# Performance work log

Measured on AMD Instinct MI355X. Metric: run time of the kernel, lower is better.

Reference implementation:

```python
import jax, jax.numpy as jnp
import numpy as np

NUM_CATEGORIES = 64
INPUT_DIM = 256
HIDDEN_DIM = 256
N = 4096  # number of samples (each with its own category)
M = 16    # rows per sample


def setup_inputs() -> dict:
    key = jax.random.key(0)
    k_x, k_cat, k_W = jax.random.split(key, 3)
    x = jax.random.normal(k_x, (N, M, INPUT_DIM), dtype=jnp.float32)
    cat_ids = jax.random.randint(k_cat, (N,), 0, NUM_CATEGORIES, dtype=jnp.int64)
    W = 0.02 * jax.random.normal(k_W, (NUM_CATEGORIES, INPUT_DIM, HIDDEN_DIM), dtype=jnp.float32)
    b = jnp.zeros((NUM_CATEGORIES, HIDDEN_DIM), dtype=jnp.float32)
    return {"x": x, "cat_ids": cat_ids, "W": W, "b": b}


def reference(x, cat_ids, W, b):
    # Gather per-sample weights/biases, then batched matmul + bias add.
    selected_W = W[cat_ids]              # [N, input_dim, hidden_dim]
    selected_b = b[cat_ids]              # [N, hidden_dim]
    out = jnp.einsum('nmi,nih->nmh', x, selected_W) + selected_b[:, None, :]
    return out
```

## Files before the change

### kernel.cpp

```cpp
#include <hip/hip_runtime.h>
#include <hip/hip_bf16.h>
#include <stdint.h>

#define N_SAMPLES 4096
#define M_ROWS 16
#define K_DIM 256
#define H_DIM 256
#define N_CATS 64
#define SPB 4
#define MAX_PADDED (N_SAMPLES + N_CATS * (SPB - 1))
#define NB (MAX_PADDED / SPB)

typedef _Float16 half8 __attribute__((ext_vector_type(8)));
typedef float floatx4 __attribute__((ext_vector_type(4)));

#define WT_BYTES ((size_t)N_CATS * K_DIM * H_DIM * 2)
#define CNT_OFF  WT_BYTES
#define CUR_OFF  (CNT_OFF + 256)
#define POFF_OFF (CNT_OFF + 512)
#define ORD_OFF  (CNT_OFF + 1024)
#define WS_NEED  (ORD_OFF + (size_t)MAX_PADDED * 4)

__global__ void prep_init(int* cnt, int* cur, int* ord) {
  int i = blockIdx.x * 256 + threadIdx.x;
  if (i < N_CATS) { cnt[i] = 0; cur[i] = 0; }
  if (i < MAX_PADDED) ord[i] = -1;
}

__global__ void prep_hist(const int* __restrict__ cat, int* cnt) {
  int i = blockIdx.x * 256 + threadIdx.x;
  if (i < N_SAMPLES) atomicAdd(&cnt[cat[i]], 1);
}

__global__ void prep_scan(const int* __restrict__ cnt, int* poff) {
  if (threadIdx.x == 0) {
    int run = 0;
    for (int c = 0; c < N_CATS; c++) {
      poff[c] = run;
      run += ((cnt[c] + SPB - 1) / SPB) * SPB;
    }
    poff[N_CATS] = run;
  }
}

__global__ void prep_scatter(const int* __restrict__ cat, const int* __restrict__ poff,
                             int* cur, int* __restrict__ ord) {
  int i = blockIdx.x * 256 + threadIdx.x;
  if (i < N_SAMPLES) {
    int c = cat[i];
    int p = poff[c] + atomicAdd(&cur[c], 1);
    ord[p] = i;
  }
}

__global__ __launch_bounds__(256)
void wt_transpose(const float* __restrict__ W, _Float16* __restrict__ Wt) {
  __shared__ _Float16 t[64][72];
  const int bid = blockIdx.x;
  const int c  = bid >> 4;
  const int kb = (bid >> 2) & 3;
  const int hb = bid & 3;
  const int tid = threadIdx.x;
  const int r  = tid >> 2;
  const int cg = (tid & 3) * 16;
  const float* src = W + ((size_t)c << 16) + (size_t)(kb * 64 + r) * 256 + hb * 64 + cg;
#pragma unroll
  for (int j = 0; j < 16; j += 4) {
    float4 v = *(const float4*)(src + j);
    t[r][cg + j + 0] = (_Float16)v.x;
    t[r][cg + j + 1] = (_Float16)v.y;
    t[r][cg + j + 2] = (_Float16)v.z;
    t[r][cg + j + 3] = (_Float16)v.w;
  }
  __syncthreads();
  _Float16* dst = Wt + ((size_t)c << 16) + (size_t)(hb * 64 + r) * 256 + kb * 64 + cg;
  half8 o0, o1;
#pragma unroll
  for (int j = 0; j < 8; j++) o0[j] = t[cg + j][r];
#pragma unroll
  for (int j = 0; j < 8; j++) o1[j] = t[cg + 8 + j][r];
  *(half8*)(dst) = o0;
  *(half8*)(dst + 8) = o1;
}

__global__ __launch_bounds__(256, 4)
void gemm_kernel(const float* __restrict__ x, const int* __restrict__ cat_ids,
                 const float* __restrict__ bias, const _Float16* __restrict__ Wt,
                 const int* __restrict__ ord, float* __restrict__ out) {
  __shared__ _Float16 sA[64 * 32];
  __shared__ _Float16 sB[H_DIM * 32];
  __shared__ int s_meta[SPB];

  const int tid = threadIdx.x;
  const int b = blockIdx.x;
  if (tid < SPB) s_meta[tid] = ord[b * SPB + tid];
  __syncthreads();
  const int s0 = s_meta[0];
  if (s0 < 0) return;
  const int cat = cat_ids[s0];

  const int wid  = tid >> 6;
  const int lane = tid & 63;
  const int l15  = lane & 15;
  const int quad = lane >> 4;

  const int arow = tid >> 2;
  const int akq  = tid & 3;
  const int asmp = s_meta[arow >> 4];
  const float* asrc = (asmp >= 0)
      ? (x + ((size_t)asmp * 16 + (arow & 15)) * K_DIM + akq * 8) : nullptr;
  _Float16* adst = &sA[arow * 32 + akq * 8];

  const _Float16* wbase = Wt + ((size_t)cat << 16);

  floatx4 acc[4][4];
#pragma unroll
  for (int i = 0; i < 4; i++)
#pragma unroll
    for (int j = 0; j < 4; j++)
#pragma unroll
      for (int e = 0; e < 4; e++) acc[i][j][e] = 0.0f;

  for (int kt = 0; kt < K_DIM / 32; ++kt) {
    __syncthreads();
    if (asrc) {
      const float4* p = (const float4*)(asrc + kt * 32);
      float4 v0 = p[0], v1 = p[1];
      half8 h;
      h[0] = (_Float16)v0.x; h[1] = (_Float16)v0.y;
      h[2] = (_Float16)v0.z; h[3] = (_Float16)v0.w;
      h[4] = (_Float16)v1.x; h[5] = (_Float16)v1.y;
      h[6] = (_Float16)v1.z; h[7] = (_Float16)v1.w;
      *(half8*)adst = h;
    } else {
      half8 h;
#pragma unroll
      for (int j = 0; j < 8; j++) h[j] = (_Float16)0.0f;
      *(half8*)adst = h;
    }
#pragma unroll
    for (int i = 0; i < 4; i++) {
      const int hbase = (wid * 4 + i) * 16;
      const _Float16* g = wbase + (size_t)(hbase + (lane >> 2)) * K_DIM + kt * 32 + (lane & 3) * 8;
      __builtin_amdgcn_global_load_lds(
          (__attribute__((address_space(1))) void*)g,
          (__attribute__((address_space(3))) void*)&sB[hbase * 32], 16, 0, 0);
    }
    __syncthreads();
    half8 af[4], bf[4];
#pragma unroll
    for (int mt = 0; mt < 4; mt++)
      af[mt] = *(const half8*)&sA[(mt * 16 + l15) * 32 + quad * 8];
#pragma unroll
    for (int nt = 0; nt < 4; nt++)
      bf[nt] = *(const half8*)&sB[(wid * 64 + nt * 16 + l15) * 32 + quad * 8];
#pragma unroll
    for (int mt = 0; mt < 4; mt++)
#pragma unroll
      for (int nt = 0; nt < 4; nt++)
        acc[mt][nt] = __builtin_amdgcn_mfma_f32_16x16x32_f16(af[mt], bf[nt], acc[mt][nt], 0, 0, 0);
  }

#pragma unroll
  for (int mt = 0; mt < 4; mt++) {
    int s = s_meta[mt];
    if (s < 0) continue;
    float* obase = out + (size_t)s * 16 * H_DIM;
#pragma unroll
    for (int nt = 0; nt < 4; nt++) {
      int col = wid * 64 + nt * 16 + l15;
      float bv = bias[cat * H_DIM + col];
#pragma unroll
      for (int r = 0; r < 4; r++) {
        int row = quad * 4 + r;
        obase[(size_t)row * H_DIM + col] = acc[mt][nt][r] + bv;
      }
    }
  }
}

__global__ __launch_bounds__(256)
void naive_kernel(const float* __restrict__ x, const int* __restrict__ cat,
                  const float* __restrict__ W, const float* __restrict__ bias,
                  float* __restrict__ out) {
  __shared__ float sx[16 * 256];
  const int n = blockIdx.x;
  const int tid = threadIdx.x;
  const int c = cat[n];
  const float* xs = x + (size_t)n * 16 * 256;
  for (int i = tid; i < 16 * 256; i += 256) sx[i] = xs[i];
  __syncthreads();
  const float* Wc = W + ((size_t)c << 16);
  float accv[16];
  float bv = bias[c * 256 + tid];
#pragma unroll
  for (int m = 0; m < 16; m++) accv[m] = bv;
  for (int k = 0; k < 256; k++) {
    float w = Wc[(size_t)k * 256 + tid];
#pragma unroll
    for (int m = 0; m < 16; m++) accv[m] += sx[m * 256 + k] * w;
  }
#pragma unroll
  for (int m = 0; m < 16; m++) out[((size_t)n * 16 + m) * 256 + tid] = accv[m];
}

extern "C" void kernel_launch(void* const* d_in, const int* in_sizes, int n_in,
                              void* d_out, int out_size, void* d_ws, size_t ws_size,
                              hipStream_t stream) {
  const float* x    = (const float*)d_in[0];
  const int*   cat  = (const int*)d_in[1];
  const float* W    = (const float*)d_in[2];
  const float* bias = (const float*)d_in[3];
  float* out = (float*)d_out;

  if (ws_size < WS_NEED) {
    naive_kernel<<<N_SAMPLES, 256, 0, stream>>>(x, cat, W, bias, out);
    return;
  }

  char* ws = (char*)d_ws;
  _Float16* Wt = (_Float16*)ws;
  int* cnt  = (int*)(ws + CNT_OFF);
  int* cur  = (int*)(ws + CUR_OFF);
  int* poff = (int*)(ws + POFF_OFF);
  int* ord  = (int*)(ws + ORD_OFF);

  wt_transpose<<<N_CATS * 16, 256, 0, stream>>>(W, Wt);
  prep_init<<<(MAX_PADDED + 255) / 256, 256, 0, stream>>>(cnt, cur, ord);
  prep_hist<<<(N_SAMPLES + 255) / 256, 256, 0, stream>>>(cat, cnt);
  prep_scan<<<1, 64, 0, stream>>>(cnt, poff);
  prep_scatter<<<(N_SAMPLES + 255) / 256, 256, 0, stream>>>(cat, poff, cur, ord);
  gemm_kernel<<<NB, 256, 0, stream>>>(x, cat, bias, Wt, ord, out);
}
```

Before: 186.1 us.

## Fuse prep kernels into one launch and split GEMM output columns across blocks

```diff
diff --git a/kernel.cpp b/kernel.cpp
--- a/kernel.cpp
+++ b/kernel.cpp
@@ -9,91 +9,90 @@
 #define N_CATS 64
 #define SPB 4
 #define MAX_PADDED (N_SAMPLES + N_CATS * (SPB - 1))
-#define NB (MAX_PADDED / SPB)
+#define NGROUP (MAX_PADDED / SPB)
+#define GPX (NGROUP / 8)
+#define GEMM_GRID (NGROUP * 2)
 
 typedef _Float16 half8 __attribute__((ext_vector_type(8)));
 typedef float floatx4 __attribute__((ext_vector_type(4)));
 
 #define WT_BYTES ((size_t)N_CATS * K_DIM * H_DIM * 2)
-#define CNT_OFF  WT_BYTES
-#define CUR_OFF  (CNT_OFF + 256)
-#define POFF_OFF (CNT_OFF + 512)
-#define ORD_OFF  (CNT_OFF + 1024)
+#define ORD_OFF  WT_BYTES
 #define WS_NEED  (ORD_OFF + (size_t)MAX_PADDED * 4)
 
-__global__ void prep_init(int* cnt, int* cur, int* ord) {
-  int i = blockIdx.x * 256 + threadIdx.x;
-  if (i < N_CATS) { cnt[i] = 0; cur[i] = 0; }
-  if (i < MAX_PADDED) ord[i] = -1;
-}
-
-__global__ void prep_hist(const int* __restrict__ cat, int* cnt) {
-  int i = blockIdx.x * 256 + threadIdx.x;
-  if (i < N_SAMPLES) atomicAdd(&cnt[cat[i]], 1);
-}
-
-__global__ void prep_scan(const int* __restrict__ cnt, int* poff) {
-  if (threadIdx.x == 0) {
-    int run = 0;
-    for (int c = 0; c < N_CATS; c++) {
-      poff[c] = run;
-      run += ((cnt[c] + SPB - 1) / SPB) * SPB;
-    }
-    poff[N_CATS] = run;
-  }
-}
-
-__global__ void prep_scatter(const int* __restrict__ cat, const int* __restrict__ poff,
-                             int* cur, int* __restrict__ ord) {
-  int i = blockIdx.x * 256 + threadIdx.x;
-  if (i < N_SAMPLES) {
-    int c = cat[i];
-    int p = poff[c] + atomicAdd(&cur[c], 1);
-    ord[p] = i;
-  }
-}
-
 __global__ __launch_bounds__(256)
-void wt_transpose(const float* __restrict__ W, _Float16* __restrict__ Wt) {
-  __shared__ _Float16 t[64][72];
-  const int bid = blockIdx.x;
-  const int c  = bid >> 4;
-  const int kb = (bid >> 2) & 3;
-  const int hb = bid & 3;
+void prep_combined(const float* __restrict__ W, _Float16* __restrict__ Wt,
+                   const int* __restrict__ cat, int* __restrict__ ord) {
   const int tid = threadIdx.x;
-  const int r  = tid >> 2;
-  const int cg = (tid & 3) * 16;
-  const float* src = W + ((size_t)c << 16) + (size_t)(kb * 64 + r) * 256 + hb * 64 + cg;
-#pragma unroll
-  for (int j = 0; j < 16; j += 4) {
-    float4 v = *(const float4*)(src + j);
-    t[r][cg + j + 0] = (_Float16)v.x;
-    t[r][cg + j + 1] = (_Float16)v.y;
-    t[r][cg + j + 2] = (_Float16)v.z;
-    t[r][cg + j + 3] = (_Float16)v.w;
-  }
-  __syncthreads();
-  _Float16* dst = Wt + ((size_t)c << 16) + (size_t)(hb * 64 + r) * 256 + kb * 64 + cg;
-  half8 o0, o1;
-#pragma unroll
-  for (int j = 0; j < 8; j++) o0[j] = t[cg + j][r];
-#pragma unroll
-  for (int j = 0; j < 8; j++) o1[j] = t[cg + 8 + j][r];
-  *(half8*)(dst) = o0;
-  *(half8*)(dst + 8) = o1;
-}
-
-__global__ __launch_bounds__(256, 4)
+  if (blockIdx.x < 1024) {
+    __shared__ _Float16 t[64][72];
+    const int bid = blockIdx.x;
+    const int c  = bid >> 4;
+    const int kb = (bid >> 2) & 3;
+    const int hb = bid & 3;
+    const int r  = tid >> 2;
+    const int cg = (tid & 3) * 16;
+    const float* src = W + ((size_t)c << 16) + (size_t)(kb * 64 + r) * 256 + hb * 64 + cg;
+#pragma unroll
+    for (int j = 0; j < 16; j += 4) {
+      float4 v = *(const float4*)(src + j);
+      t[r][cg + j + 0] = (_Float16)v.x;
+      t[r][cg + j + 1] = (_Float16)v.y;
+      t[r][cg + j + 2] = (_Float16)v.z;
+      t[r][cg + j + 3] = (_Float16)v.w;
+    }
+    __syncthreads();
+    _Float16* dst = Wt + ((size_t)c << 16) + (size_t)(hb * 64 + r) * 256 + kb * 64 + cg;
+    half8 o0, o1;
+#pragma unroll
+    for (int j = 0; j < 8; j++) o0[j] = t[cg + j][r];
+#pragma unroll
+    for (int j = 0; j < 8; j++) o1[j] = t[cg + 8 + j][r];
+    *(half8*)(dst) = o0;
+    *(half8*)(dst + 8) = o1;
+  } else {
+    __shared__ int hist[N_CATS];
+    __shared__ int poffs[N_CATS];
+    __shared__ int curs[N_CATS];
+    if (tid < N_CATS) hist[tid] = 0;
+    for (int i = tid; i < MAX_PADDED; i += 256) ord[i] = -1;
+    __syncthreads();
+    for (int i = tid; i < N_SAMPLES; i += 256) atomicAdd(&hist[cat[i]], 1);
+    __syncthreads();
+    if (tid == 0) {
+      int run = 0;
+      for (int c = 0; c < N_CATS; c++) {
+        poffs[c] = run;
+        run += ((hist[c] + SPB - 1) / SPB) * SPB;
+      }
+    }
+    if (tid < N_CATS) curs[tid] = 0;
+    __syncthreads();
+    for (int i = tid; i < N_SAMPLES; i += 256) {
+      int c = cat[i];
+      int p = poffs[c] + atomicAdd(&curs[c], 1);
+      ord[p] = i;
+    }
+  }
+}
+
+__global__ __launch_bounds__(256, 8)
 void gemm_kernel(const float* __restrict__ x, const int* __restrict__ cat_ids,
                  const float* __restrict__ bias, const _Float16* __restrict__ Wt,
                  const int* __restrict__ ord, float* __restrict__ out) {
   __shared__ _Float16 sA[64 * 32];
-  __shared__ _Float16 sB[H_DIM * 32];
+  __shared__ _Float16 sB[128 * 32];
   __shared__ int s_meta[SPB];
 
   const int tid = threadIdx.x;
-  const int b = blockIdx.x;
-  if (tid < SPB) s_meta[tid] = ord[b * SPB + tid];
+  const int B = blockIdx.x;
+  const int xcd = B & 7;
+  const int slot = B >> 3;
+  const int h_half = slot & 1;
+  const int group = xcd * GPX + (slot >> 1);
+  const int h0 = h_half << 7;
+
+  if (tid < SPB) s_meta[tid] = ord[group * SPB + tid];
   __syncthreads();
   const int s0 = s_meta[0];
   if (s0 < 0) return;
@@ -113,11 +112,11 @@
 
   const _Float16* wbase = Wt + ((size_t)cat << 16);
 
-  floatx4 acc[4][4];
+  floatx4 acc[4][2];
 #pragma unroll
   for (int i = 0; i < 4; i++)
 #pragma unroll
-    for (int j = 0; j < 4; j++)
+    for (int j = 0; j < 2; j++)
 #pragma unroll
       for (int e = 0; e < 4; e++) acc[i][j][e] = 0.0f;
 
@@ -139,25 +138,25 @@
       *(half8*)adst = h;
     }
 #pragma unroll
-    for (int i = 0; i < 4; i++) {
-      const int hbase = (wid * 4 + i) * 16;
-      const _Float16* g = wbase + (size_t)(hbase + (lane >> 2)) * K_DIM + kt * 32 + (lane & 3) * 8;
+    for (int j = 0; j < 2; j++) {
+      const int hloc = wid * 16 + 64 * j;
+      const _Float16* g = wbase + (size_t)(h0 + hloc + (lane >> 2)) * K_DIM + kt * 32 + (lane & 3) * 8;
       __builtin_amdgcn_global_load_lds(
           (__attribute__((address_space(1))) void*)g,
-          (__attribute__((address_space(3))) void*)&sB[hbase * 32], 16, 0, 0);
-    }
-    __syncthreads();
-    half8 af[4], bf[4];
+          (__attribute__((address_space(3))) void*)&sB[hloc * 32], 16, 0, 0);
+    }
+    __syncthreads();
+    half8 af[4], bf[2];
 #pragma unroll
     for (int mt = 0; mt < 4; mt++)
       af[mt] = *(const half8*)&sA[(mt * 16 + l15) * 32 + quad * 8];
 #pragma unroll
-    for (int nt = 0; nt < 4; nt++)
-      bf[nt] = *(const half8*)&sB[(wid * 64 + nt * 16 + l15) * 32 + quad * 8];
+    for (int nt = 0; nt < 2; nt++)
+      bf[nt] = *(const half8*)&sB[(wid * 32 + nt * 16 + l15) * 32 + quad * 8];
 #pragma unroll
     for (int mt = 0; mt < 4; mt++)
 #pragma unroll
-      for (int nt = 0; nt < 4; nt++)
+      for (int nt = 0; nt < 2; nt++)
         acc[mt][nt] = __builtin_amdgcn_mfma_f32_16x16x32_f16(af[mt], bf[nt], acc[mt][nt], 0, 0, 0);
   }
 
@@ -167,8 +166,8 @@
     if (s < 0) continue;
     float* obase = out + (size_t)s * 16 * H_DIM;
 #pragma unroll
-    for (int nt = 0; nt < 4; nt++) {
-      int col = wid * 64 + nt * 16 + l15;
+    for (int nt = 0; nt < 2; nt++) {
+      int col = h0 + wid * 32 + nt * 16 + l15;
       float bv = bias[cat * H_DIM + col];
 #pragma unroll
       for (int r = 0; r < 4; r++) {
@@ -220,15 +219,8 @@
 
   char* ws = (char*)d_ws;
   _Float16* Wt = (_Float16*)ws;
-  int* cnt  = (int*)(ws + CNT_OFF);
-  int* cur  = (int*)(ws + CUR_OFF);
-  int* poff = (int*)(ws + POFF_OFF);
-  int* ord  = (int*)(ws + ORD_OFF);
-
-  wt_transpose<<<N_CATS * 16, 256, 0, stream>>>(W, Wt);
-  prep_init<<<(MAX_PADDED + 255) / 256, 256, 0, stream>>>(cnt, cur, ord);
-  prep_hist<<<(N_SAMPLES + 255) / 256, 256, 0, stream>>>(cat, cnt);
-  prep_scan<<<1, 64, 0, stream>>>(cnt, poff);
-  prep_scatter<<<(N_SAMPLES + 255) / 256, 256, 0, stream>>>(cat, poff, cur, ord);
-  gemm_kernel<<<NB, 256, 0, stream>>>(x, cat, bias, Wt, ord, out);
-}
+  int* ord = (int*)(ws + ORD_OFF);
+
+  prep_combined<<<1025, 256, 0, stream>>>(W, Wt, cat, ord);
+  gemm_kernel<<<GEMM_GRID, 256, 0, stream>>>(x, cat, bias, Wt, ord, out);
+}
```

Result: faster. 176.6 us (-5.1%).
